# Kernel tuning notes

Hardware: AMD Instinct MI355X
Metric: run time of the kernel (lower is better)

The kernel has to match this reference:

```python
import jax, jax.numpy as jnp
import numpy as np

_HMT = np.array([[1, 1, 1, 1], [1, -1, 1, -1], [1, 1, -1, -1], [1, -1, -1, 1]], dtype=np.float32)
_H = jnp.asarray(_HMT)
_H2 = jnp.asarray(_HMT[[1, 0, 2, 3], :])
_H3 = jnp.asarray(_HMT[[3, 1, 2, 0], :])
# inverse-transform rows 1:3 (2x4), reconstructed from truncated source
_IH = _H[1:3, :]
_IH2 = _H2[1:3, :]
_IH3 = _H3[1:3, :]

KERNEL = 4
STRIDE = 2


def setup_inputs() -> dict:
    key = jax.random.key(0)
    k1, k2, k3 = jax.random.split(key, 3)
    B, Cin, Cout, ih, iw = 16, 64, 96, 128, 128
    x = jax.random.normal(k1, (B, Cin, ih, iw), dtype=jnp.float32)
    weight = jax.random.normal(k2, (Cout, Cin, KERNEL, KERNEL), dtype=jnp.float32) * 0.05
    bias = jax.random.normal(k3, (1, Cout, 1, 1), dtype=jnp.float32) * 0.05
    return {"x": x, "weight": weight, "bias": bias}


def _extract_patches(xp, nH, nW):
    # patches[b,c,i,j,u,v] = xp[b,c, 2i+v, 2j+u]  (torch unfold(3).unfold(2) order)
    idx_h = 2 * np.arange(nH)[:, None] + np.arange(KERNEL)[None, :]  # (nH,4) over (i,v)
    idx_w = 2 * np.arange(nW)[:, None] + np.arange(KERNEL)[None, :]  # (nW,4) over (j,u)
    return xp[:, :, idx_h[:, None, None, :], idx_w[None, :, :, None]]  # (B,C,nH,nW,4,4)


def _group(t, w, ih_mat):
    # t: (B,C,nH,nW,4,4) transform-domain patches; w: (Og,C,4,4)
    m = jnp.einsum('bcijuv,ocuv->boijuv', t, w)
    # IH @ m @ IH.T -> (B,Og,nH,nW,2,2)
    return jnp.einsum('pu,boijuv,qv->boijpq', ih_mat, m, ih_mat)


def reference(x, weight, bias):
    B, Cin, ih, iw = x.shape
    Cout = weight.shape[0]
    nH, nW = ih // STRIDE, iw // STRIDE
    xp = jnp.pad(x, ((0, 0), (0, 0), (1, 1), (1, 1)))
    patches = _extract_patches(xp, nH, nW)
    # forward transforms: H @ P @ H ; H2.T @ P @ H2 ; H3.T @ P @ H3
    t1 = jnp.einsum('au,bcijuv,vd->bcijad', _H, patches, _H)
    t2 = jnp.einsum('ua,bcijuv,vd->bcijad', _H2, patches, _H2)
    t3 = jnp.einsum('ua,bcijuv,vd->bcijad', _H3, patches, _H3)
    g = Cout // 3
    h1 = _group(t1, weight[:g], _IH)
    h2 = _group(t2, weight[g:2 * g], _IH2)
    h3 = _group(t3, weight[2 * g:], _IH3)
    hmult = jnp.concatenate([h1, h2, h3], axis=1)  # (B,Cout,nH,nW,2,2)
    # out[b,o,2i+p,2j+q] = hmult[b,o,i,j,p,q]
    out = hmult.transpose(0, 1, 2, 4, 3, 5).reshape(B, Cout, ih, iw)
    return out + bias
```

## Files before the change

### kernel.cpp

```cpp
#include <hip/hip_runtime.h>
#include <hip/hip_bf16.h>
#include <cstddef>
#include <cstdint>


#define IHW 128
#define CIN 64
#define COUT 96
#define NCK 16
#define P_DW 168
#define COFF_DW 80
#define XBUF_DW (12 * P_DW)
#define ABUF_DW 4096

typedef __attribute__((ext_vector_type(8))) short short8_t;
typedef __attribute__((ext_vector_type(4))) float floatx4;

__device__ __forceinline__ short bf16r(float f) {
  uint32_t u = __float_as_uint(f);
  uint32_t r = (u + 0x7FFFu + ((u >> 16) & 1u)) >> 16;
  return (short)r;
}

__device__ __forceinline__ uint32_t pk(float lo, float hi) {
  union { __hip_bfloat16 h; unsigned short s; } a, bq;
  a.h = __float2bfloat16(lo);
  bq.h = __float2bfloat16(hi);
  return (uint32_t)a.s | ((uint32_t)bq.s << 16);
}

__global__ void keff_kernel(const float* __restrict__ w, short* __restrict__ keff) {
  int idx = blockIdx.x * 256 + threadIdx.x;
  if (idx >= COUT * CIN) return;
  int o = idx / CIN, c = idx % CIN;
  int g = o / 32;

  int perm[4] = {0, 1, 2, 3};
  if (g == 1) { perm[0] = 1; perm[1] = 0; }
  else if (g == 2) { perm[0] = 3; perm[3] = 0; }

  const float H[4][4] = {{1,1,1,1},{1,-1,1,-1},{1,1,-1,-1},{1,-1,-1,1}};
  float S[2][4];
#pragma unroll
  for (int p = 0; p < 2; ++p)
#pragma unroll
    for (int a = 0; a < 4; ++a) {
      bool pos = (g == 1) ? ((p == 0) ? true : (a < 2))
                          : ((p == 0) ? ((a & 1) == 0) : (a < 2));
      S[p][a] = pos ? 1.f : -1.f;
    }

  float wv[4][4];
#pragma unroll
  for (int a = 0; a < 4; ++a)
#pragma unroll
    for (int d = 0; d < 4; ++d) wv[a][d] = w[(o * CIN + c) * 16 + a * 4 + d];

  for (int p = 0; p < 2; ++p)
    for (int q = 0; q < 2; ++q) {
      int n = o * 4 + p * 2 + q;
      for (int y = 0; y < 4; ++y)
        for (int xx = 0; xx < 4; ++xx) {
          float s = 0.f;
#pragma unroll
          for (int a = 0; a < 4; ++a) {
            float ea = S[p][a] * H[a][perm[xx]];
#pragma unroll
            for (int d = 0; d < 4; ++d) s += ea * S[q][d] * H[d][perm[y]] * wv[a][d];
          }
          keff[n * 1024 + c * 16 + y * 4 + xx] = bf16r(s);
        }
    }
}

__global__ __launch_bounds__(256) void conv_mfma(const float* __restrict__ x,
                                                 const short* __restrict__ keff,
                                                 const float* __restrict__ bias,
                                                 float* __restrict__ out) {
  __shared__ uint32_t xlds[2 * XBUF_DW];
  __shared__ uint32_t alds[2 * ABUF_DW];

  const int tid = threadIdx.x;
  const int lane = tid & 63;
  const int wid = tid >> 6;
  const int wavem = wid >> 1;
  const int wn = wid & 1;
  const int l15 = lane & 15;
  const int l4 = lane >> 4;

  const int hw = blockIdx.x;
  const int xcd = hw & 7;
  const int r = hw >> 3;
  const int tile = xcd * 64 + r / 3;
  const int nblk = r % 3;
  const int b = tile >> 5;
  const int ib = tile & 31;
  const int gy0 = ib * 4 - 1;

  const float* xb = x + (size_t)b * CIN * IHW * IHW;

  int sl_off[3], sl_dw[3], sl_s[3];
  bool sl_ok[3];
#pragma unroll
  for (int it = 0; it < 3; ++it) {
    const int slot = tid + it * 256;
    const int seg = slot >> 5;
    const int s = slot & 31;
    const int c_sub = seg / 12;
    const int rr = seg % 12;
    const int kk2 = rr / 6;
    const int y = rr % 6;
    const int c_loc = 2 * kk2 + c_sub;
    const int gy = gy0 + y;
    const bool ok = (unsigned)gy < (unsigned)IHW;
    sl_off[it] = (c_loc * IHW + (ok ? gy : 0)) * IHW + 4 * s;
    sl_dw[it] = rr * P_DW + c_sub * COFF_DW;
    sl_s[it] = s;
    sl_ok[it] = ok;
  }

  int aoff[4];
#pragma unroll
  for (int it = 0; it < 4; ++it) {
    const int slot = tid + it * 256;
    const int n = slot >> 3;
    const int u = slot & 7;
    aoff[it] = (nblk * 128 + n) * 1024 + ((u ^ (n & 7)) << 3);
  }

  float4 gv[3];
  float gn[3];
#define ISSUE(ckv)                                                        \
  {                                                                       \
    _Pragma("unroll") for (int it = 0; it < 3; ++it) {                    \
      const float* p = xb + sl_off[it] + (size_t)(ckv) * (4 * IHW * IHW); \
      gv[it] = *reinterpret_cast<const float4*>(p);                       \
      gn[it] = (sl_s[it] < 31) ? p[4] : 0.f;                              \
    }                                                                     \
  }

#define WRITEST(bs)                                                       \
  {                                                                       \
    uint32_t* Bp = xlds + (bs) * XBUF_DW;                                 \
    _Pragma("unroll") for (int it = 0; it < 3; ++it) {                    \
      float4 v = gv[it];                                                  \
      float nx = gn[it];                                                  \
      if (!sl_ok[it]) { v.x = 0.f; v.y = 0.f; v.z = 0.f; v.w = 0.f; nx = 0.f; } \
      const int o = sl_dw[it] + 2 * sl_s[it] + 1;                         \
      Bp[o] = pk(v.y, v.z);                                               \
      Bp[o + 1] = pk(v.w, nx);                                            \
      if (sl_s[it] == 0) Bp[sl_dw[it]] = pk(0.f, v.x);                    \
    }                                                                     \
  }

#define ADMA(bs, ckv)                                                     \
  {                                                                       \
    _Pragma("unroll") for (int it = 0; it < 4; ++it) {                    \
      const short* src = keff + aoff[it] + (ckv) * 64;                    \
      __builtin_amdgcn_global_load_lds(                                   \
          (const __attribute__((address_space(1))) void*)src,             \
          (__attribute__((address_space(3))) void*)                       \
              &alds[(bs) * ABUF_DW + (tid + it * 256) * 4],               \
          16, 0, 0);                                                      \
    }                                                                     \
  }

#define COMPUTE(ckv)                                                      \
  {                                                                       \
    const uint32_t* Xp = xlds + ((ckv) & 1) * XBUF_DW;                    \
    const uint32_t* Ap = alds + ((ckv) & 1) * ABUF_DW;                    \
    _Pragma("unroll") for (int kk = 0; kk < 2; ++kk) {                    \
      short8_t af[4];                                                     \
      _Pragma("unroll") for (int nf = 0; nf < 4; ++nf) {                  \
        const int row = wn * 64 + nf * 16 + l15;                          \
        const int off = row * 32 + ((((kk << 2) | l4) ^ (l15 & 7)) << 2); \
        af[nf] = *reinterpret_cast<const short8_t*>(Ap + off);            \
      }                                                                   \
      const int od = cm_dw + kk * (6 * P_DW);                             \
      _Pragma("unroll") for (int mf = 0; mf < 4; ++mf) {                  \
        const int o = od + mf * 16;                                       \
        union { short8_t s8; uint32_t u[4]; } frag;                       \
        frag.u[0] = Xp[o];                                                \
        frag.u[1] = Xp[o + 1];                                            \
        frag.u[2] = Xp[o + P_DW];                                         \
        frag.u[3] = Xp[o + P_DW + 1];                                     \
        _Pragma("unroll") for (int nf = 0; nf < 4; ++nf)                  \
          acc[mf][nf] = __builtin_amdgcn_mfma_f32_16x16x32_bf16(          \
              af[nf], frag.s8, acc[mf][nf], 0, 0, 0);                     \
      }                                                                   \
    }                                                                     \
  }

  floatx4 acc[4][4];
#pragma unroll
  for (int i = 0; i < 4; ++i)
#pragma unroll
    for (int j2 = 0; j2 < 4; ++j2) acc[i][j2] = (floatx4){0.f, 0.f, 0.f, 0.f};

  float biasr[4];
#pragma unroll
  for (int nf = 0; nf < 4; ++nf) biasr[nf] = bias[nblk * 32 + wn * 16 + nf * 4 + l4];

  const int cm_dw = (2 * wavem + 2 * (l4 & 1)) * P_DW + (l4 >> 1) * COFF_DW + l15;

  ISSUE(0);
  ADMA(0, 0);
  __builtin_amdgcn_sched_barrier(0);
  WRITEST(0);
  ISSUE(1);

  for (int ck = 0; ck < NCK - 1; ++ck) {
    asm volatile("s_waitcnt vmcnt(6) lgkmcnt(0)" ::: "memory");
    __builtin_amdgcn_s_barrier();
    __builtin_amdgcn_sched_barrier(0);

    const int nb = (ck + 1) & 1;
    ADMA(nb, ck + 1);
    __builtin_amdgcn_sched_barrier(0);
    WRITEST(nb);
    if (ck + 2 < NCK) ISSUE(ck + 2);
    COMPUTE(ck);
  }

  asm volatile("s_waitcnt vmcnt(0) lgkmcnt(0)" ::: "memory");
  __builtin_amdgcn_s_barrier();
  __builtin_amdgcn_sched_barrier(0);
  COMPUTE(NCK - 1);

  const int i_row = ib * 2 + wavem;
  const int orow0 = 2 * i_row;
#pragma unroll
  for (int nf = 0; nf < 4; ++nf) {
    const int o = nblk * 32 + wn * 16 + nf * 4 + l4;
    const float bv = biasr[nf];
    float* obase = out + ((size_t)(b * COUT + o) * IHW + orow0) * IHW;
#pragma unroll
    for (int mf = 0; mf < 4; ++mf) {
      const int col = 2 * (mf * 16 + l15);
      float2 s0 = make_float2(acc[mf][nf][0] + bv, acc[mf][nf][1] + bv);
      float2 s1 = make_float2(acc[mf][nf][2] + bv, acc[mf][nf][3] + bv);
      *reinterpret_cast<float2*>(obase + col) = s0;
      *reinterpret_cast<float2*>(obase + IHW + col) = s1;
    }
  }
#undef ISSUE
#undef WRITEST
#undef ADMA
#undef COMPUTE
}

extern "C" void kernel_launch(void* const* d_in, const int* in_sizes, int n_in,
                              void* d_out, int out_size, void* d_ws, size_t ws_size,
                              hipStream_t stream) {
  const float* x = (const float*)d_in[0];
  const float* w = (const float*)d_in[1];
  const float* bias = (const float*)d_in[2];
  float* out = (float*)d_out;
  short* keff = (short*)d_ws;

  hipLaunchKernelGGL(keff_kernel, dim3(24), dim3(256), 0, stream, w, keff);
  hipLaunchKernelGGL(conv_mfma, dim3(1536), dim3(256), 0, stream, x, keff, bias, out);
}
```

Measured before the change: 78.98 us.

## Reorder main loop to run MFMAs before LDS staging writes, add setprio

Splits the compute macro into per-k steps and places both MFMA steps before the LDS staging writes in each loop iteration, so global loads have more time to land before their data is written into the next buffer. The A-fragment addresses are hoisted into two precomputed offsets, and each step gathers all fragments before issuing 16 MFMAs in a block wrapped in s_setprio. Several sched_barriers are removed, which gives the compiler more freedom but makes the instruction order less predictable.

```diff
diff --git a/kernel.cpp b/kernel.cpp
--- a/kernel.cpp
+++ b/kernel.cpp
@@ -165,30 +165,26 @@
     }                                                                     \
   }
 
-#define COMPUTE(ckv)                                                      \
-  {                                                                       \
-    const uint32_t* Xp = xlds + ((ckv) & 1) * XBUF_DW;                    \
-    const uint32_t* Ap = alds + ((ckv) & 1) * ABUF_DW;                    \
-    _Pragma("unroll") for (int kk = 0; kk < 2; ++kk) {                    \
-      short8_t af[4];                                                     \
-      _Pragma("unroll") for (int nf = 0; nf < 4; ++nf) {                  \
-        const int row = wn * 64 + nf * 16 + l15;                          \
-        const int off = row * 32 + ((((kk << 2) | l4) ^ (l15 & 7)) << 2); \
-        af[nf] = *reinterpret_cast<const short8_t*>(Ap + off);            \
-      }                                                                   \
-      const int od = cm_dw + kk * (6 * P_DW);                             \
-      _Pragma("unroll") for (int mf = 0; mf < 4; ++mf) {                  \
-        const int o = od + mf * 16;                                       \
-        union { short8_t s8; uint32_t u[4]; } frag;                       \
-        frag.u[0] = Xp[o];                                                \
-        frag.u[1] = Xp[o + 1];                                            \
-        frag.u[2] = Xp[o + P_DW];                                         \
-        frag.u[3] = Xp[o + P_DW + 1];                                     \
-        _Pragma("unroll") for (int nf = 0; nf < 4; ++nf)                  \
-          acc[mf][nf] = __builtin_amdgcn_mfma_f32_16x16x32_bf16(          \
-              af[nf], frag.s8, acc[mf][nf], 0, 0, 0);                     \
-      }                                                                   \
-    }                                                                     \
+  union ufrag { short8_t s8; uint32_t u[4]; };
+
+#define KKSTEP(Apt, Xkt, abase)                                           \
+  {                                                                       \
+    short8_t af[4];                                                       \
+    _Pragma("unroll") for (int nf = 0; nf < 4; ++nf)                      \
+      af[nf] = *reinterpret_cast<const short8_t*>((Apt) + (abase) + nf * 512); \
+    ufrag xf[4];                                                          \
+    _Pragma("unroll") for (int mf = 0; mf < 4; ++mf) {                    \
+      xf[mf].u[0] = (Xkt)[mf * 16];                                       \
+      xf[mf].u[1] = (Xkt)[mf * 16 + 1];                                   \
+      xf[mf].u[2] = (Xkt)[mf * 16 + P_DW];                                \
+      xf[mf].u[3] = (Xkt)[mf * 16 + P_DW + 1];                            \
+    }                                                                     \
+    __builtin_amdgcn_s_setprio(1);                                        \
+    _Pragma("unroll") for (int mf = 0; mf < 4; ++mf)                      \
+      _Pragma("unroll") for (int nf = 0; nf < 4; ++nf)                    \
+        acc[mf][nf] = __builtin_amdgcn_mfma_f32_16x16x32_bf16(            \
+            af[nf], xf[mf].s8, acc[mf][nf], 0, 0, 0);                     \
+    __builtin_amdgcn_s_setprio(0);                                        \
   }
 
   floatx4 acc[4][4];
@@ -202,10 +198,11 @@
   for (int nf = 0; nf < 4; ++nf) biasr[nf] = bias[nblk * 32 + wn * 16 + nf * 4 + l4];
 
   const int cm_dw = (2 * wavem + 2 * (l4 & 1)) * P_DW + (l4 >> 1) * COFF_DW + l15;
+  const int a0 = (wn * 64 + l15) * 32 + ((l4 ^ (l15 & 7)) << 2);
+  const int a1 = a0 ^ 16;
 
   ISSUE(0);
   ADMA(0, 0);
-  __builtin_amdgcn_sched_barrier(0);
   WRITEST(0);
   ISSUE(1);
 
@@ -214,18 +211,28 @@
     __builtin_amdgcn_s_barrier();
     __builtin_amdgcn_sched_barrier(0);
 
-    const int nb = (ck + 1) & 1;
-    ADMA(nb, ck + 1);
-    __builtin_amdgcn_sched_barrier(0);
-    WRITEST(nb);
+    const int cur = ck & 1;
+    const uint32_t* Ap = alds + cur * ABUF_DW;
+    const uint32_t* Xk0 = xlds + cur * XBUF_DW + cm_dw;
+    const uint32_t* Xk1 = Xk0 + 6 * P_DW;
+
+    ADMA(cur ^ 1, ck + 1);
+    KKSTEP(Ap, Xk0, a0);
+    KKSTEP(Ap, Xk1, a1);
+    WRITEST(cur ^ 1);
     if (ck + 2 < NCK) ISSUE(ck + 2);
-    COMPUTE(ck);
   }
 
   asm volatile("s_waitcnt vmcnt(0) lgkmcnt(0)" ::: "memory");
   __builtin_amdgcn_s_barrier();
   __builtin_amdgcn_sched_barrier(0);
-  COMPUTE(NCK - 1);
+  {
+    const uint32_t* Ap = alds + ABUF_DW;
+    const uint32_t* Xk0 = xlds + XBUF_DW + cm_dw;
+    const uint32_t* Xk1 = Xk0 + 6 * P_DW;
+    KKSTEP(Ap, Xk0, a0);
+    KKSTEP(Ap, Xk1, a1);
+  }
 
   const int i_row = ib * 2 + wavem;
   const int orow0 = 2 * i_row;
@@ -246,7 +253,7 @@
 #undef ISSUE
 #undef WRITEST
 #undef ADMA
-#undef COMPUTE
+#undef KKSTEP
 }
 
 extern "C" void kernel_launch(void* const* d_in, const int* in_sizes, int n_in,
```

Measured after the change: 81.75 us. +3.5%, slower.

## Halve M-tile to one output row pair, single-buffer weights, add setprio

Applied to the files above, without the earlier changes.

Each block now covers one output row pair (half the previous M tile), so the grid doubles and the accumulators per wave halve. The weight tile is single-buffered in LDS with an extra barrier, so compute now runs before the next DMA and staging. MFMA sections are wrapped in s_setprio. The aim is higher occupancy and less LDS per block, at the cost of more redundant halo-row loads and weight reloads per output, plus less overlap between loads and compute.

```diff
diff --git a/kernel.cpp b/kernel.cpp
--- a/kernel.cpp
+++ b/kernel.cpp
@@ -8,9 +8,9 @@
 #define CIN 64
 #define COUT 96
 #define NCK 16
-#define P_DW 168
+#define P_DW 152
 #define COFF_DW 80
-#define XBUF_DW (12 * P_DW)
+#define XBUF_DW (8 * P_DW)
 #define ABUF_DW 4096
 
 typedef __attribute__((ext_vector_type(8))) short short8_t;
@@ -78,7 +78,7 @@
                                                  const float* __restrict__ bias,
                                                  float* __restrict__ out) {
   __shared__ uint32_t xlds[2 * XBUF_DW];
-  __shared__ uint32_t alds[2 * ABUF_DW];
+  __shared__ uint32_t alds[ABUF_DW];
 
   const int tid = threadIdx.x;
   const int lane = tid & 63;
@@ -91,30 +91,26 @@
   const int hw = blockIdx.x;
   const int xcd = hw & 7;
   const int r = hw >> 3;
-  const int tile = xcd * 64 + r / 3;
+  const int mtile = xcd * 128 + r / 3;
   const int nblk = r % 3;
-  const int b = tile >> 5;
-  const int ib = tile & 31;
-  const int gy0 = ib * 4 - 1;
+  const int b = mtile >> 6;
+  const int i = mtile & 63;
+  const int gy0 = 2 * i - 1;
 
   const float* xb = x + (size_t)b * CIN * IHW * IHW;
 
-  int sl_off[3], sl_dw[3], sl_s[3];
-  bool sl_ok[3];
-#pragma unroll
-  for (int it = 0; it < 3; ++it) {
+  int sl_off[2], sl_dw[2], sl_s[2];
+  bool sl_ok[2];
+#pragma unroll
+  for (int it = 0; it < 2; ++it) {
     const int slot = tid + it * 256;
-    const int seg = slot >> 5;
+    const int c_loc = slot >> 7;
+    const int y = (slot >> 5) & 3;
     const int s = slot & 31;
-    const int c_sub = seg / 12;
-    const int rr = seg % 12;
-    const int kk2 = rr / 6;
-    const int y = rr % 6;
-    const int c_loc = 2 * kk2 + c_sub;
     const int gy = gy0 + y;
     const bool ok = (unsigned)gy < (unsigned)IHW;
     sl_off[it] = (c_loc * IHW + (ok ? gy : 0)) * IHW + 4 * s;
-    sl_dw[it] = rr * P_DW + c_sub * COFF_DW;
+    sl_dw[it] = ((c_loc >> 1) * 4 + y) * P_DW + (c_loc & 1) * COFF_DW;
     sl_s[it] = s;
     sl_ok[it] = ok;
   }
@@ -128,11 +124,11 @@
     aoff[it] = (nblk * 128 + n) * 1024 + ((u ^ (n & 7)) << 3);
   }
 
-  float4 gv[3];
-  float gn[3];
+  float4 gv[2];
+  float gn[2];
 #define ISSUE(ckv)                                                        \
   {                                                                       \
-    _Pragma("unroll") for (int it = 0; it < 3; ++it) {                    \
+    _Pragma("unroll") for (int it = 0; it < 2; ++it) {                    \
       const float* p = xb + sl_off[it] + (size_t)(ckv) * (4 * IHW * IHW); \
       gv[it] = *reinterpret_cast<const float4*>(p);                       \
       gn[it] = (sl_s[it] < 31) ? p[4] : 0.f;                              \
@@ -142,7 +138,7 @@
 #define WRITEST(bs)                                                       \
   {                                                                       \
     uint32_t* Bp = xlds + (bs) * XBUF_DW;                                 \
-    _Pragma("unroll") for (int it = 0; it < 3; ++it) {                    \
+    _Pragma("unroll") for (int it = 0; it < 2; ++it) {                    \
       float4 v = gv[it];                                                  \
       float nx = gn[it];                                                  \
       if (!sl_ok[it]) { v.x = 0.f; v.y = 0.f; v.z = 0.f; v.w = 0.f; nx = 0.f; } \
@@ -153,73 +149,77 @@
     }                                                                     \
   }
 
-#define ADMA(bs, ckv)                                                     \
+#define ADMA(ckv)                                                         \
   {                                                                       \
     _Pragma("unroll") for (int it = 0; it < 4; ++it) {                    \
       const short* src = keff + aoff[it] + (ckv) * 64;                    \
       __builtin_amdgcn_global_load_lds(                                   \
           (const __attribute__((address_space(1))) void*)src,             \
           (__attribute__((address_space(3))) void*)                       \
-              &alds[(bs) * ABUF_DW + (tid + it * 256) * 4],               \
+              &alds[(tid + it * 256) * 4],                                \
           16, 0, 0);                                                      \
     }                                                                     \
   }
 
+  union ufrag { short8_t s8; uint32_t u[4]; };
+
 #define COMPUTE(ckv)                                                      \
   {                                                                       \
     const uint32_t* Xp = xlds + ((ckv) & 1) * XBUF_DW;                    \
-    const uint32_t* Ap = alds + ((ckv) & 1) * ABUF_DW;                    \
     _Pragma("unroll") for (int kk = 0; kk < 2; ++kk) {                    \
       short8_t af[4];                                                     \
       _Pragma("unroll") for (int nf = 0; nf < 4; ++nf) {                  \
         const int row = wn * 64 + nf * 16 + l15;                          \
         const int off = row * 32 + ((((kk << 2) | l4) ^ (l15 & 7)) << 2); \
-        af[nf] = *reinterpret_cast<const short8_t*>(Ap + off);            \
+        af[nf] = *reinterpret_cast<const short8_t*>(alds + off);          \
       }                                                                   \
-      const int od = cm_dw + kk * (6 * P_DW);                             \
-      _Pragma("unroll") for (int mf = 0; mf < 4; ++mf) {                  \
+      const int od = cm_dw + kk * (4 * P_DW);                             \
+      ufrag xf[2];                                                        \
+      _Pragma("unroll") for (int mf = 0; mf < 2; ++mf) {                  \
         const int o = od + mf * 16;                                       \
-        union { short8_t s8; uint32_t u[4]; } frag;                       \
-        frag.u[0] = Xp[o];                                                \
-        frag.u[1] = Xp[o + 1];                                            \
-        frag.u[2] = Xp[o + P_DW];                                         \
-        frag.u[3] = Xp[o + P_DW + 1];                                     \
+        xf[mf].u[0] = Xp[o];                                              \
+        xf[mf].u[1] = Xp[o + 1];                                          \
+        xf[mf].u[2] = Xp[o + P_DW];                                       \
+        xf[mf].u[3] = Xp[o + P_DW + 1];                                   \
+      }                                                                   \
+      __builtin_amdgcn_s_setprio(1);                                      \
+      _Pragma("unroll") for (int mf = 0; mf < 2; ++mf)                    \
         _Pragma("unroll") for (int nf = 0; nf < 4; ++nf)                  \
           acc[mf][nf] = __builtin_amdgcn_mfma_f32_16x16x32_bf16(          \
-              af[nf], frag.s8, acc[mf][nf], 0, 0, 0);                     \
-      }                                                                   \
-    }                                                                     \
-  }
-
-  floatx4 acc[4][4];
-#pragma unroll
-  for (int i = 0; i < 4; ++i)
-#pragma unroll
-    for (int j2 = 0; j2 < 4; ++j2) acc[i][j2] = (floatx4){0.f, 0.f, 0.f, 0.f};
+              af[nf], xf[mf].s8, acc[mf][nf], 0, 0, 0);                   \
+      __builtin_amdgcn_s_setprio(0);                                      \
+    }                                                                     \
+  }
+
+  floatx4 acc[2][4];
+#pragma unroll
+  for (int i2 = 0; i2 < 2; ++i2)
+#pragma unroll
+    for (int j2 = 0; j2 < 4; ++j2) acc[i2][j2] = (floatx4){0.f, 0.f, 0.f, 0.f};
 
   float biasr[4];
 #pragma unroll
   for (int nf = 0; nf < 4; ++nf) biasr[nf] = bias[nblk * 32 + wn * 16 + nf * 4 + l4];
 
-  const int cm_dw = (2 * wavem + 2 * (l4 & 1)) * P_DW + (l4 >> 1) * COFF_DW + l15;
+  const int cm_dw = (2 * (l4 & 1)) * P_DW + (l4 >> 1) * COFF_DW + wavem * 32 + l15;
 
   ISSUE(0);
-  ADMA(0, 0);
-  __builtin_amdgcn_sched_barrier(0);
+  ADMA(0);
   WRITEST(0);
   ISSUE(1);
 
   for (int ck = 0; ck < NCK - 1; ++ck) {
-    asm volatile("s_waitcnt vmcnt(6) lgkmcnt(0)" ::: "memory");
+    asm volatile("s_waitcnt vmcnt(4) lgkmcnt(0)" ::: "memory");
     __builtin_amdgcn_s_barrier();
     __builtin_amdgcn_sched_barrier(0);
 
-    const int nb = (ck + 1) & 1;
-    ADMA(nb, ck + 1);
+    COMPUTE(ck);
+
+    __builtin_amdgcn_s_barrier();
     __builtin_amdgcn_sched_barrier(0);
-    WRITEST(nb);
+    ADMA(ck + 1);
+    WRITEST((ck + 1) & 1);
     if (ck + 2 < NCK) ISSUE(ck + 2);
-    COMPUTE(ck);
   }
 
   asm volatile("s_waitcnt vmcnt(0) lgkmcnt(0)" ::: "memory");
@@ -227,16 +227,15 @@
   __builtin_amdgcn_sched_barrier(0);
   COMPUTE(NCK - 1);
 
-  const int i_row = ib * 2 + wavem;
-  const int orow0 = 2 * i_row;
+  const int orow0 = 2 * i;
 #pragma unroll
   for (int nf = 0; nf < 4; ++nf) {
     const int o = nblk * 32 + wn * 16 + nf * 4 + l4;
     const float bv = biasr[nf];
     float* obase = out + ((size_t)(b * COUT + o) * IHW + orow0) * IHW;
 #pragma unroll
-    for (int mf = 0; mf < 4; ++mf) {
-      const int col = 2 * (mf * 16 + l15);
+    for (int mf = 0; mf < 2; ++mf) {
+      const int col = 2 * (wavem * 32 + mf * 16 + l15);
       float2 s0 = make_float2(acc[mf][nf][0] + bv, acc[mf][nf][1] + bv);
       float2 s1 = make_float2(acc[mf][nf][2] + bv, acc[mf][nf][3] + bv);
       *reinterpret_cast<float2*>(obase + col) = s0;
@@ -259,5 +258,5 @@
   short* keff = (short*)d_ws;
 
   hipLaunchKernelGGL(keff_kernel, dim3(24), dim3(256), 0, stream, w, keff);
-  hipLaunchKernelGGL(conv_mfma, dim3(1536), dim3(256), 0, stream, x, keff, bias, out);
-}
+  hipLaunchKernelGGL(conv_mfma, dim3(3072), dim3(256), 0, stream, x, keff, bias, out);
+}
```

New measurement: 93.67 us. 1.19x slower.
